# Optimization experiments

Measured on AMD Instinct MI355X. Metric: run time of the kernel, lower is better.

The kernel has to match this reference:

```python
import jax, jax.numpy as jnp
import numpy as np

N = 20000          # nodes
E = 200000         # edges
IN = 256           # in_channels
OUT = 256          # out_channels (heads * per-head)
H = 2              # heads
C = OUT // 2       # per-head channels (out_channels // 2)
TDIM = 100         # time_enc.out_channels
MSG = 156          # msg_dim
EDGE_DIM = TDIM + MSG  # 256
P = 0.1            # dropout prob


def setup_inputs() -> dict:
    key = jax.random.key(0)
    ks = jax.random.split(key, 20)
    s = 1.0 / np.sqrt(IN)
    se = 1.0 / np.sqrt(EDGE_DIM)
    return {
        "x": jax.random.normal(ks[0], (N, IN), jnp.float32),
        "last_update": jax.random.uniform(ks[1], (N,), jnp.float32) * 100.0,
        "edge_index": jax.random.randint(ks[2], (2, E), 0, N, jnp.int64),
        "t": jax.random.uniform(ks[3], (E,), jnp.float32) * 100.0,
        "msg": jax.random.normal(ks[4], (E, MSG), jnp.float32),
        "u_edge": jax.random.uniform(ks[5], (E,), jnp.float32),
        "u_attn": jax.random.uniform(ks[6], (E, H), jnp.float32),
        # TimeEncoder: cos(Linear(1, TDIM))
        "time_w": jax.random.normal(ks[7], (TDIM,), jnp.float32),
        "time_b": jax.random.normal(ks[8], (TDIM,), jnp.float32) * 0.1,
        # TransformerConv params ([in, out] layout)
        "Wq": jax.random.normal(ks[9], (IN, H * C), jnp.float32) * s,
        "bq": jnp.zeros((H * C,), jnp.float32),
        "Wk": jax.random.normal(ks[10], (IN, H * C), jnp.float32) * s,
        "bk": jnp.zeros((H * C,), jnp.float32),
        "Wv": jax.random.normal(ks[11], (IN, H * C), jnp.float32) * s,
        "bv": jnp.zeros((H * C,), jnp.float32),
        "We": jax.random.normal(ks[12], (EDGE_DIM, H * C), jnp.float32) * se,
        "be": jnp.zeros((H * C,), jnp.float32),
        "Ws": jax.random.normal(ks[13], (IN, H * C), jnp.float32) * s,
        "bs": jnp.zeros((H * C,), jnp.float32),
    }


def reference(x, last_update, edge_index, t, msg, u_edge, u_attn,
              time_w, time_b, Wq, bq, Wk, bk, Wv, bv, We, be, Ws, bs):
    src, dst = edge_index[0], edge_index[1]
    # time encoding of relative time (TGN TimeEncoder: cos(Linear(1, TDIM)))
    rel_t = last_update[src] - t                              # [E]
    rel_enc = jnp.cos(rel_t[:, None] * time_w[None, :] + time_b)  # [E, TDIM]
    edge_attr = jnp.concatenate([rel_enc, msg], axis=-1)      # [E, EDGE_DIM]
    # dropout_adj: drop edges with prob P (no rescale)
    keep = u_edge > P                                         # [E] bool

    q = (x @ Wq + bq).reshape(N, H, C)
    k = (x @ Wk + bk).reshape(N, H, C)
    v = (x @ Wv + bv).reshape(N, H, C)
    e = (edge_attr @ We + be).reshape(E, H, C)

    kj = k[src] + e                                           # [E, H, C]
    alpha = jnp.einsum('ehc,ehc->eh', q[dst], kj) / jnp.sqrt(jnp.float32(C))
    alpha = jnp.where(keep[:, None], alpha, -jnp.inf)
    # segment softmax over incoming edges of each dst node
    m = jax.ops.segment_max(alpha, dst, num_segments=N)       # [N, H]
    m = jnp.where(jnp.isfinite(m), m, 0.0)
    ex = jnp.where(keep[:, None], jnp.exp(alpha - m[dst]), 0.0)
    denom = jax.ops.segment_sum(ex, dst, num_segments=N)      # [N, H]
    attn = ex / (denom[dst] + 1e-16)                          # [E, H]
    # attention dropout (post-softmax, inverted scaling)
    attn = attn * (u_attn > P).astype(attn.dtype) / (1.0 - P)

    msg_out = (v[src] + e) * attn[:, :, None]                 # [E, H, C]
    out = jax.ops.segment_sum(msg_out, dst, num_segments=N).reshape(N, H * C)
    # root/skip connection
    return out + (x @ Ws + bs)
```

## Files before the change

### kernel.cpp

```cpp
#include <hip/hip_runtime.h>

#define NND 20000
#define NE 200000
#define PDROP 0.1f

typedef unsigned short u16;
typedef __bf16 bf16x8 __attribute__((ext_vector_type(8)));
typedef float f32x4 __attribute__((ext_vector_type(4)));

__device__ __forceinline__ float b2f(u16 u) {
  unsigned v = ((unsigned)u) << 16;
  float f;
  __builtin_memcpy(&f, &v, 4);
  return f;
}
__device__ __forceinline__ u16 f2b(float f) {
  unsigned x;
  __builtin_memcpy(&x, &f, 4);
  unsigned r = x + 0x7fffu + ((x >> 16) & 1u);
  return (u16)(r >> 16);
}

struct WTArgs {
  const float* W[6];
  u16* WT[6];
};

__global__ __launch_bounds__(256) void prep(const float* __restrict__ x,
                                            u16* __restrict__ xb, WTArgs a,
                                            int* __restrict__ cnt,
                                            int* __restrict__ cur) {
  const int b = blockIdx.x, tid = threadIdx.x;
  if (b < 5000) {
    int i = b * 256 + tid;
    float4 v = ((const float4*)x)[i];
    ushort4 o;
    o.x = f2b(v.x); o.y = f2b(v.y); o.z = f2b(v.z); o.w = f2b(v.w);
    ((ushort4*)xb)[i] = o;
  } else if (b < 6536) {
    int gid = (b - 5000) * 256 + tid;
    int w = gid >> 16, r = gid & 65535;
    if (w < 5) {
      int n = r >> 8, k = r & 255;
      a.WT[w][n * 256 + k] = f2b(a.W[w][k * 256 + n]);
    } else {
      a.WT[5][r] = f2b(a.W[5][r]);
    }
  } else {
    int i = (b - 6536) * 256 + tid;
    if (i < NND) { cnt[i] = 0; cur[i] = 0; }
  }
}

__global__ void csr_count(const int* __restrict__ ei, int* __restrict__ cnt) {
  int e = blockIdx.x * blockDim.x + threadIdx.x;
  if (e < NE) atomicAdd(&cnt[ei[NE + e]], 1);
}
__global__ __launch_bounds__(1024) void scan_rowptr(const int* __restrict__ cnt,
                                                    int* __restrict__ rowptr) {
  __shared__ int sums[1024];
  const int tid = threadIdx.x;
  const int base = tid * 20;
  int local[20];
  int run = 0;
#pragma unroll
  for (int i = 0; i < 20; i++) {
    int idx = base + i;
    local[i] = run;
    run += (idx < NND) ? cnt[idx] : 0;
  }
  sums[tid] = run;
  __syncthreads();
  for (int off = 1; off < 1024; off <<= 1) {
    int v = (tid >= off) ? sums[tid - off] : 0;
    __syncthreads();
    sums[tid] += v;
    __syncthreads();
  }
  int prev = (tid > 0) ? sums[tid - 1] : 0;
#pragma unroll
  for (int i = 0; i < 20; i++) {
    int idx = base + i;
    if (idx < NND) rowptr[idx] = prev + local[i];
  }
  if (tid == 1023) rowptr[NND] = sums[1023];
}

__global__ __launch_bounds__(256) void csr_fill(
    const int* __restrict__ ei, const float* __restrict__ last_update,
    const float* __restrict__ t, const float* __restrict__ u_edge,
    const float* __restrict__ u_attn, const float* __restrict__ msg,
    const int* __restrict__ rowptr, int* __restrict__ cur,
    uint4* __restrict__ recs, u16* __restrict__ msgs) {
  int e = (blockIdx.x * blockDim.x + threadIdx.x) >> 6;
  int lane = threadIdx.x & 63;
  if (e >= NE) return;
  int p = 0;
  if (lane == 0) {
    int s = ei[e];
    int d = ei[NE + e];
    p = rowptr[d] + atomicAdd(&cur[d], 1);
    bool keep = u_edge[e] > PDROP;
    float rt = last_update[s] - t[e];
    float2 ua = *(const float2*)&u_attn[(size_t)e * 2];
    uint4 r;
    r.x = (unsigned)s | (keep ? 0u : 0x80000000u);
    r.y = __float_as_uint(rt);
    r.z = __float_as_uint(ua.x > PDROP ? (1.f / 0.9f) : 0.f);
    r.w = __float_as_uint(ua.y > PDROP ? (1.f / 0.9f) : 0.f);
    recs[p] = r;
  }
  p = __shfl(p, 0);
  int c = lane * 4;
  if (c < 156) {
    float4 v = *(const float4*)&msg[(size_t)e * 156 + c];
    ushort4 o;
    o.x = f2b(v.x); o.y = f2b(v.y); o.z = f2b(v.z); o.w = f2b(v.w);
    *(ushort4*)&msgs[(size_t)p * 156 + c] = o;
  }
}

__device__ __forceinline__ void mfma_tile(const u16 (*As)[72], const u16 (*Bs)[72],
                                          f32x4 acc[4][4], int wm, int wn,
                                          int fr, int fg) {
#pragma unroll
  for (int ks = 0; ks < 2; ks++) {
    bf16x8 a[4], b[4];
#pragma unroll
    for (int i = 0; i < 4; i++)
      a[i] = *(const bf16x8*)&As[wm * 64 + i * 16 + fr][ks * 32 + fg * 8];
#pragma unroll
    for (int j = 0; j < 4; j++)
      b[j] = *(const bf16x8*)&Bs[wn * 64 + j * 16 + fr][ks * 32 + fg * 8];
#pragma unroll
    for (int i = 0; i < 4; i++)
#pragma unroll
      for (int j = 0; j < 4; j++)
        acc[i][j] = __builtin_amdgcn_mfma_f32_16x16x32_bf16(a[i], b[j], acc[i][j], 0, 0, 0);
  }
}

struct NodeArgs {
  const u16* BT[4];
  const float* bias[4];
  u16* outb[3];
  float* outf;
};
__global__ __launch_bounds__(256) void gemm_node(const u16* __restrict__ xb,
                                                 NodeArgs args) {
  __shared__ __attribute__((aligned(16))) u16 As[128][72];
  __shared__ __attribute__((aligned(16))) u16 Bs[128][72];
  const int tid = threadIdx.x;
  const int w = blockIdx.y >> 1;
  const int col0 = (blockIdx.y & 1) * 128;
  const int row0 = blockIdx.x * 128;
  const u16* BT = args.BT[w];
  const float* bias = args.bias[w];
  const int wid = tid >> 6, lane = tid & 63;
  const int wm = wid >> 1, wn = wid & 1;
  const int fr = lane & 15, fg = lane >> 4;
  f32x4 acc[4][4] = {};
  for (int k0 = 0; k0 < 256; k0 += 64) {
#pragma unroll
    for (int i = 0; i < 4; i++) {
      int idx = tid + i * 256;
      int row = idx >> 3, vc = idx & 7;
      int g = row0 + row;
      uint4 v = make_uint4(0, 0, 0, 0);
      if (g < NND) v = *(const uint4*)&xb[(size_t)g * 256 + k0 + vc * 8];
      *(uint4*)&As[row][vc * 8] = v;
      *(uint4*)&Bs[row][vc * 8] = *(const uint4*)&BT[(size_t)(col0 + row) * 256 + k0 + vc * 8];
    }
    __syncthreads();
    mfma_tile(As, Bs, acc, wm, wn, fr, fg);
    __syncthreads();
  }
#pragma unroll
  for (int mi = 0; mi < 4; mi++) {
#pragma unroll
    for (int rr = 0; rr < 4; rr++) {
      int grow = row0 + wm * 64 + mi * 16 + fg * 4 + rr;
      if (grow >= NND) continue;
#pragma unroll
      for (int ni = 0; ni < 4; ni++) {
        int gcol = col0 + wn * 64 + ni * 16 + fr;
        float val = acc[mi][ni][rr] + bias[gcol];
        if (w < 3)
          args.outb[w][(size_t)grow * 256 + gcol] = f2b(val);
        else
          args.outf[(size_t)grow * 256 + gcol] = val;
      }
    }
  }
}

__global__ __launch_bounds__(256) void gemm_qwe(const u16* __restrict__ qb,
                                                const u16* __restrict__ Web,
                                                u16* __restrict__ qWeb) {
  __shared__ __attribute__((aligned(16))) u16 As[128][72];
  __shared__ __attribute__((aligned(16))) u16 Bs[128][72];
  const int tid = threadIdx.x;
  const int h = blockIdx.y >> 1;
  const int col0 = (blockIdx.y & 1) * 128;
  const int row0 = blockIdx.x * 128;
  const int wid = tid >> 6, lane = tid & 63;
  const int wm = wid >> 1, wn = wid & 1;
  const int fr = lane & 15, fg = lane >> 4;
  f32x4 acc[4][4] = {};
  for (int k0 = 0; k0 < 128; k0 += 64) {
#pragma unroll
    for (int i = 0; i < 4; i++) {
      int idx = tid + i * 256;
      int row = idx >> 3, vc = idx & 7;
      int g = row0 + row;
      uint4 v = make_uint4(0, 0, 0, 0);
      if (g < NND) v = *(const uint4*)&qb[(size_t)g * 256 + h * 128 + k0 + vc * 8];
      *(uint4*)&As[row][vc * 8] = v;
      *(uint4*)&Bs[row][vc * 8] =
          *(const uint4*)&Web[(size_t)(col0 + row) * 256 + h * 128 + k0 + vc * 8];
    }
    __syncthreads();
    mfma_tile(As, Bs, acc, wm, wn, fr, fg);
    __syncthreads();
  }
#pragma unroll
  for (int mi = 0; mi < 4; mi++) {
#pragma unroll
    for (int rr = 0; rr < 4; rr++) {
      int grow = row0 + wm * 64 + mi * 16 + fg * 4 + rr;
      if (grow >= NND) continue;
#pragma unroll
      for (int ni = 0; ni < 4; ni++) {
        int gj = col0 + wn * 64 + ni * 16 + fr;
        qWeb[(size_t)grow * 512 + h * 256 + gj] = f2b(acc[mi][ni][rr]);
      }
    }
  }
}

__global__ __launch_bounds__(256) void node_fused(
    const u16* __restrict__ qb, const u16* __restrict__ kb,
    const u16* __restrict__ vb, const u16* __restrict__ qWeb,
    const u16* __restrict__ msgs, const float* __restrict__ tw,
    const float* __restrict__ tb_, const float* __restrict__ be,
    const int* __restrict__ rowptr, const uint4* __restrict__ recs,
    u16* __restrict__ aggb, float* __restrict__ out) {
  const int node = (blockIdx.x * blockDim.x + threadIdx.x) >> 6;
  const int lane = threadIdx.x & 63;
  if (node >= NND) return;
  const int beg = rowptr[node], end = rowptr[node + 1];
  const int c0 = lane * 4, hl = lane >> 5;

  ushort4 q4 = *(const ushort4*)&qb[(size_t)node * 256 + c0];
  float qf0 = b2f(q4.x), qf1 = b2f(q4.y), qf2 = b2f(q4.z), qf3 = b2f(q4.w);
  ushort4 w0v = *(const ushort4*)&qWeb[(size_t)node * 512 + c0];
  ushort4 w1v = *(const ushort4*)&qWeb[(size_t)node * 512 + 256 + c0];
  float qw00 = b2f(w0v.x), qw01 = b2f(w0v.y), qw02 = b2f(w0v.z), qw03 = b2f(w0v.w);
  float qw10 = b2f(w1v.x), qw11 = b2f(w1v.y), qw12 = b2f(w1v.z), qw13 = b2f(w1v.w);
  float4 bev = *(const float4*)&be[c0];
  float pb = qf0 * bev.x + qf1 * bev.y + qf2 * bev.z + qf3 * bev.w;
#pragma unroll
  for (int off = 16; off; off >>= 1) pb += __shfl_xor(pb, off);
  float tw0 = 0, tw1 = 0, tw2 = 0, tw3 = 0, tb0 = 0, tb1 = 0, tb2 = 0, tb3 = 0;
  if (c0 < 100) {
    float4 a = *(const float4*)&tw[c0];
    float4 b = *(const float4*)&tb_[c0];
    tw0 = a.x; tw1 = a.y; tw2 = a.z; tw3 = a.w;
    tb0 = b.x; tb1 = b.y; tb2 = b.z; tb3 = b.w;
  }
  const float inv = 0.08838834764831845f;

  float m0 = -INFINITY, m1 = -INFINITY;
  float den0 = 0.f, den1 = 0.f, sw0 = 0.f, sw1 = 0.f;
  float vc0 = 0, vc1 = 0, vc2 = 0, vc3 = 0;
  float g00 = 0, g01 = 0, g02 = 0, g03 = 0;
  float g10 = 0, g11 = 0, g12 = 0, g13 = 0;

  for (int j0 = beg; j0 < end; j0 += 4) {
    float ea[4][4];
    unsigned se[4];
    float rt[4], wk0[4], wk1[4];
    ushort4 k4[4], v4[4], mm4[4];
#pragma unroll
    for (int e = 0; e < 4; ++e) {
      int j = j0 + e;
      int jc = (j < end) ? j : (end - 1);
      uint4 rr = recs[jc];
      bool valid = (j < end);
      se[e] = valid ? rr.x : 0xFFFFFFFFu;
      rt[e] = __uint_as_float(rr.y);
      wk0[e] = valid ? __uint_as_float(rr.z) : 0.f;
      wk1[e] = valid ? __uint_as_float(rr.w) : 0.f;
      int s_ = (int)(rr.x & 0x7fffffffu);
      k4[e] = *(const ushort4*)&kb[(size_t)s_ * 256 + c0];
      v4[e] = *(const ushort4*)&vb[(size_t)s_ * 256 + c0];
      if (c0 >= 100)
        mm4[e] = *(const ushort4*)&msgs[(size_t)jc * 156 + (c0 - 100)];
    }
    if (c0 < 100) {
#pragma unroll
      for (int e = 0; e < 4; ++e) {
        ea[e][0] = __cosf(rt[e] * tw0 + tb0);
        ea[e][1] = __cosf(rt[e] * tw1 + tb1);
        ea[e][2] = __cosf(rt[e] * tw2 + tb2);
        ea[e][3] = __cosf(rt[e] * tw3 + tb3);
      }
    } else {
#pragma unroll
      for (int e = 0; e < 4; ++e) {
        ea[e][0] = b2f(mm4[e].x); ea[e][1] = b2f(mm4[e].y);
        ea[e][2] = b2f(mm4[e].z); ea[e][3] = b2f(mm4[e].w);
      }
    }
    float zq[4];
#pragma unroll
    for (int e = 0; e < 4; ++e) {
      float pq = qf0 * b2f(k4[e].x) + qf1 * b2f(k4[e].y) +
                 qf2 * b2f(k4[e].z) + qf3 * b2f(k4[e].w);
      float pe0 = qw00 * ea[e][0] + qw01 * ea[e][1] + qw02 * ea[e][2] + qw03 * ea[e][3];
      float pe1 = qw10 * ea[e][0] + qw11 * ea[e][1] + qw12 * ea[e][2] + qw13 * ea[e][3];
      float y0 = pe0 + __shfl_xor(pe0, 32);
      float y1 = pe1 + __shfl_xor(pe1, 32);
      zq[e] = ((lane < 32) ? y0 : y1) + pq;
    }
#pragma unroll
    for (int off = 16; off; off >>= 1) {
#pragma unroll
      for (int e = 0; e < 4; ++e) zq[e] += __shfl_xor(zq[e], off);
    }
    float a0[4], a1[4];
#pragma unroll
    for (int e = 0; e < 4; ++e) {
      float a = (se[e] < 0x80000000u) ? (zq[e] + pb) * inv : -INFINITY;
      float aoth = __shfl_xor(a, 32);
      a0[e] = (lane < 32) ? a : aoth;
      a1[e] = (lane < 32) ? aoth : a;
    }
    float cm0 = fmaxf(fmaxf(a0[0], a0[1]), fmaxf(a0[2], a0[3]));
    float cm1 = fmaxf(fmaxf(a1[0], a1[1]), fmaxf(a1[2], a1[3]));
    if (cm0 > m0) {
      float sc = (m0 > -1e30f) ? __expf(m0 - cm0) : 0.f;
      den0 *= sc; sw0 *= sc;
      g00 *= sc; g01 *= sc; g02 *= sc; g03 *= sc;
      float scv = hl ? 1.f : sc;
      vc0 *= scv; vc1 *= scv; vc2 *= scv; vc3 *= scv;
      m0 = cm0;
    }
    if (cm1 > m1) {
      float sc = (m1 > -1e30f) ? __expf(m1 - cm1) : 0.f;
      den1 *= sc; sw1 *= sc;
      g10 *= sc; g11 *= sc; g12 *= sc; g13 *= sc;
      float scv = hl ? sc : 1.f;
      vc0 *= scv; vc1 *= scv; vc2 *= scv; vc3 *= scv;
      m1 = cm1;
    }
#pragma unroll
    for (int e = 0; e < 4; ++e) {
      float ex0 = (a0[e] > -1e30f) ? __expf(a0[e] - m0) : 0.f;
      float ex1 = (a1[e] > -1e30f) ? __expf(a1[e] - m1) : 0.f;
      den0 += ex0; den1 += ex1;
      float w0 = ex0 * wk0[e], w1 = ex1 * wk1[e];
      float wv = hl ? w1 : w0;
      vc0 += wv * b2f(v4[e].x); vc1 += wv * b2f(v4[e].y);
      vc2 += wv * b2f(v4[e].z); vc3 += wv * b2f(v4[e].w);
      g00 += w0 * ea[e][0]; g01 += w0 * ea[e][1];
      g02 += w0 * ea[e][2]; g03 += w0 * ea[e][3];
      g10 += w1 * ea[e][0]; g11 += w1 * ea[e][1];
      g12 += w1 * ea[e][2]; g13 += w1 * ea[e][3];
      sw0 += w0; sw1 += w1;
    }
  }

  float rden0 = 1.f / (den0 + 1e-16f), rden1 = 1.f / (den1 + 1e-16f);
  float rv = hl ? rden1 : rden0;
  float swv = hl ? sw1 : sw0;
  float4 o = *(float4*)&out[(size_t)node * 256 + c0];
  o.x += (vc0 + swv * bev.x) * rv;
  o.y += (vc1 + swv * bev.y) * rv;
  o.z += (vc2 + swv * bev.z) * rv;
  o.w += (vc3 + swv * bev.w) * rv;
  *(float4*)&out[(size_t)node * 256 + c0] = o;
  ushort4 a0v, a1v;
  a0v.x = f2b(g00 * rden0); a0v.y = f2b(g01 * rden0);
  a0v.z = f2b(g02 * rden0); a0v.w = f2b(g03 * rden0);
  a1v.x = f2b(g10 * rden1); a1v.y = f2b(g11 * rden1);
  a1v.z = f2b(g12 * rden1); a1v.w = f2b(g13 * rden1);
  *(ushort4*)&aggb[(size_t)node * 256 + c0] = a0v;
  *(ushort4*)&aggb[(size_t)(NND + node) * 256 + c0] = a1v;
}

__global__ __launch_bounds__(256) void gemm_final(const u16* __restrict__ aggb,
                                                  const u16* __restrict__ WeT,
                                                  float* __restrict__ out) {
  __shared__ __attribute__((aligned(16))) u16 As[128][72];
  __shared__ __attribute__((aligned(16))) u16 Bs[128][72];
  const int tid = threadIdx.x;
  const int h = blockIdx.y;
  const int row0 = blockIdx.x * 128;
  const u16* A = aggb + (size_t)h * NND * 256;
  const int wid = tid >> 6, lane = tid & 63;
  const int wm = wid >> 1, wn = wid & 1;
  const int fr = lane & 15, fg = lane >> 4;
  f32x4 acc[4][4] = {};
  for (int k0 = 0; k0 < 256; k0 += 64) {
#pragma unroll
    for (int i = 0; i < 4; i++) {
      int idx = tid + i * 256;
      int row = idx >> 3, vc = idx & 7;
      int g = row0 + row;
      uint4 v = make_uint4(0, 0, 0, 0);
      if (g < NND) v = *(const uint4*)&A[(size_t)g * 256 + k0 + vc * 8];
      *(uint4*)&As[row][vc * 8] = v;
      *(uint4*)&Bs[row][vc * 8] =
          *(const uint4*)&WeT[(size_t)(h * 128 + row) * 256 + k0 + vc * 8];
    }
    __syncthreads();
    mfma_tile(As, Bs, acc, wm, wn, fr, fg);
    __syncthreads();
  }
#pragma unroll
  for (int mi = 0; mi < 4; mi++) {
#pragma unroll
    for (int rr = 0; rr < 4; rr++) {
      int grow = row0 + wm * 64 + mi * 16 + fg * 4 + rr;
      if (grow >= NND) continue;
#pragma unroll
      for (int ni = 0; ni < 4; ni++) {
        int gcol = wn * 64 + ni * 16 + fr;
        out[(size_t)grow * 256 + h * 128 + gcol] += acc[mi][ni][rr];
      }
    }
  }
}

extern "C" void kernel_launch(void* const* d_in, const int* in_sizes, int n_in,
                              void* d_out, int out_size, void* d_ws, size_t ws_size,
                              hipStream_t stream) {
  const float* x = (const float*)d_in[0];
  const float* last_update = (const float*)d_in[1];
  const int* ei = (const int*)d_in[2];
  const float* t = (const float*)d_in[3];
  const float* msg = (const float*)d_in[4];
  const float* u_edge = (const float*)d_in[5];
  const float* u_attn = (const float*)d_in[6];
  const float* time_w = (const float*)d_in[7];
  const float* time_b = (const float*)d_in[8];
  const float* Wq = (const float*)d_in[9];
  const float* bq = (const float*)d_in[10];
  const float* Wk = (const float*)d_in[11];
  const float* bk = (const float*)d_in[12];
  const float* Wv = (const float*)d_in[13];
  const float* bv = (const float*)d_in[14];
  const float* We = (const float*)d_in[15];
  const float* be = (const float*)d_in[16];
  const float* Ws = (const float*)d_in[17];
  const float* bs = (const float*)d_in[18];
  float* out = (float*)d_out;

  char* ws = (char*)d_ws;
  u16* xb = (u16*)(ws + 0);
  u16* WT0 = (u16*)(ws + 10240000);
  u16* qb = (u16*)(ws + 11026432);
  u16* kb = (u16*)(ws + 21266432);
  u16* vb = (u16*)(ws + 31506432);
  u16* qWeb = (u16*)(ws + 41746432);
  u16* aggb = (u16*)(ws + 62226432);
  uint4* recs = (uint4*)(ws + 82706432);
  u16* msgs = (u16*)(ws + 85906432);
  int* cnt = (int*)(ws + 148306432);
  int* cur = (int*)(ws + 148386432);
  int* rowptr = (int*)(ws + 148466432);

  WTArgs wa;
  wa.W[0] = Wq; wa.W[1] = Wk; wa.W[2] = Wv; wa.W[3] = Ws; wa.W[4] = We; wa.W[5] = We;
  for (int i = 0; i < 6; i++) wa.WT[i] = WT0 + (size_t)i * 65536;
  prep<<<6615, 256, 0, stream>>>(x, xb, wa, cnt, cur);

  csr_count<<<(NE + 255) / 256, 256, 0, stream>>>(ei, cnt);
  scan_rowptr<<<1, 1024, 0, stream>>>(cnt, rowptr);
  csr_fill<<<NE / 4, 256, 0, stream>>>(ei, last_update, t, u_edge, u_attn, msg,
                                       rowptr, cur, recs, msgs);

  NodeArgs na;
  na.BT[0] = wa.WT[0]; na.BT[1] = wa.WT[1]; na.BT[2] = wa.WT[2]; na.BT[3] = wa.WT[3];
  na.bias[0] = bq; na.bias[1] = bk; na.bias[2] = bv; na.bias[3] = bs;
  na.outb[0] = qb; na.outb[1] = kb; na.outb[2] = vb;
  na.outf = out;
  dim3 gn((NND + 127) / 128, 8);
  gemm_node<<<gn, 256, 0, stream>>>(xb, na);

  dim3 gq((NND + 127) / 128, 4);
  gemm_qwe<<<gq, 256, 0, stream>>>(qb, wa.WT[5], qWeb);

  node_fused<<<(NND + 3) / 4, 256, 0, stream>>>(
      qb, kb, vb, qWeb, msgs, time_w, time_b, be, rowptr, recs, aggb, out);

  dim3 gf((NND + 127) / 128, 2);
  gemm_final<<<gf, 256, 0, stream>>>(aggb, wa.WT[4], out);
}
```

Measured before the change: 268.5 us.

## Fold Wq·We into combined weight and convert msg in edge order

Precomputes Wq_h·We_h^T (and bq·We) as a combined weight so q·We is produced directly from x inside the node GEMM, removing the separate gemm_qwe kernel that depended on q. The msg bf16 conversion moves into a coalesced prep pass in original edge order, and the CSR records now carry the edge id so node_fused gathers msg rows by edge id. This cuts the one-warp-per-edge csr_fill scatter but makes msg reads in node_fused random instead of sequential, and adds a small weight-product kernel.

```diff
diff --git a/kernel.cpp b/kernel.cpp
--- a/kernel.cpp
+++ b/kernel.cpp
@@ -22,33 +22,62 @@
 }
 
 struct WTArgs {
-  const float* W[6];
-  u16* WT[6];
+  const float* W[5];
+  u16* WT[5];
 };
 
 __global__ __launch_bounds__(256) void prep(const float* __restrict__ x,
                                             u16* __restrict__ xb, WTArgs a,
+                                            const float* __restrict__ msg,
+                                            u16* __restrict__ msgb,
                                             int* __restrict__ cnt,
                                             int* __restrict__ cur) {
   const int b = blockIdx.x, tid = threadIdx.x;
-  if (b < 5000) {
+  if (b < 30469) {
     int i = b * 256 + tid;
+    if (i < 7800000) {
+      float4 v = ((const float4*)msg)[i];
+      ushort4 o;
+      o.x = f2b(v.x); o.y = f2b(v.y); o.z = f2b(v.z); o.w = f2b(v.w);
+      ((ushort4*)msgb)[i] = o;
+    }
+  } else if (b < 35469) {
+    int i = (b - 30469) * 256 + tid;
     float4 v = ((const float4*)x)[i];
     ushort4 o;
     o.x = f2b(v.x); o.y = f2b(v.y); o.z = f2b(v.z); o.w = f2b(v.w);
     ((ushort4*)xb)[i] = o;
-  } else if (b < 6536) {
-    int gid = (b - 5000) * 256 + tid;
+  } else if (b < 36749) {
+    int gid = (b - 35469) * 256 + tid;
     int w = gid >> 16, r = gid & 65535;
-    if (w < 5) {
-      int n = r >> 8, k = r & 255;
-      a.WT[w][n * 256 + k] = f2b(a.W[w][k * 256 + n]);
-    } else {
-      a.WT[5][r] = f2b(a.W[5][r]);
-    }
+    int n = r >> 8, k = r & 255;
+    a.WT[w][n * 256 + k] = f2b(a.W[w][k * 256 + n]);
   } else {
-    int i = (b - 6536) * 256 + tid;
+    int i = (b - 36749) * 256 + tid;
     if (i < NND) { cnt[i] = 0; cur[i] = 0; }
+  }
+}
+
+__global__ void wprep(const float* __restrict__ Wq, const float* __restrict__ We,
+                      const float* __restrict__ bq, u16* __restrict__ WcT,
+                      float* __restrict__ qwe_bias) {
+  int gid = blockIdx.x * blockDim.x + threadIdx.x;
+  if (gid < 131072) {
+    int i = gid & 255, j = gid >> 8;
+    int h = j >> 8, jj = j & 255;
+    float acc = 0.f;
+#pragma unroll 4
+    for (int c = 0; c < 128; c++)
+      acc += Wq[i * 256 + h * 128 + c] * We[jj * 256 + h * 128 + c];
+    WcT[j * 256 + i] = f2b(acc);
+  } else if (gid < 131584) {
+    int j = gid - 131072;
+    int h = j >> 8, jj = j & 255;
+    float acc = 0.f;
+#pragma unroll 4
+    for (int c = 0; c < 128; c++)
+      acc += bq[h * 128 + c] * We[jj * 256 + h * 128 + c];
+    qwe_bias[j] = acc;
   }
 }
 
@@ -86,37 +115,28 @@
   if (tid == 1023) rowptr[NND] = sums[1023];
 }
 
-__global__ __launch_bounds__(256) void csr_fill(
-    const int* __restrict__ ei, const float* __restrict__ last_update,
-    const float* __restrict__ t, const float* __restrict__ u_edge,
-    const float* __restrict__ u_attn, const float* __restrict__ msg,
-    const int* __restrict__ rowptr, int* __restrict__ cur,
-    uint4* __restrict__ recs, u16* __restrict__ msgs) {
-  int e = (blockIdx.x * blockDim.x + threadIdx.x) >> 6;
-  int lane = threadIdx.x & 63;
-  if (e >= NE) return;
-  int p = 0;
-  if (lane == 0) {
+__global__ void csr_fill(const int* __restrict__ ei,
+                         const float* __restrict__ last_update,
+                         const float* __restrict__ t,
+                         const float* __restrict__ u_edge,
+                         const float* __restrict__ u_attn,
+                         const int* __restrict__ rowptr, int* __restrict__ cur,
+                         uint4* __restrict__ recs) {
+  int e = blockIdx.x * blockDim.x + threadIdx.x;
+  if (e < NE) {
     int s = ei[e];
     int d = ei[NE + e];
-    p = rowptr[d] + atomicAdd(&cur[d], 1);
+    int p = rowptr[d] + atomicAdd(&cur[d], 1);
     bool keep = u_edge[e] > PDROP;
     float rt = last_update[s] - t[e];
     float2 ua = *(const float2*)&u_attn[(size_t)e * 2];
     uint4 r;
     r.x = (unsigned)s | (keep ? 0u : 0x80000000u);
     r.y = __float_as_uint(rt);
-    r.z = __float_as_uint(ua.x > PDROP ? (1.f / 0.9f) : 0.f);
-    r.w = __float_as_uint(ua.y > PDROP ? (1.f / 0.9f) : 0.f);
+    r.z = (unsigned)e | ((ua.x > PDROP) ? 0x40000000u : 0u) |
+          ((ua.y > PDROP) ? 0x80000000u : 0u);
+    r.w = 0u;
     recs[p] = r;
-  }
-  p = __shfl(p, 0);
-  int c = lane * 4;
-  if (c < 156) {
-    float4 v = *(const float4*)&msg[(size_t)e * 156 + c];
-    ushort4 o;
-    o.x = f2b(v.x); o.y = f2b(v.y); o.z = f2b(v.z); o.w = f2b(v.w);
-    *(ushort4*)&msgs[(size_t)p * 156 + c] = o;
   }
 }
 
@@ -141,10 +161,11 @@
 }
 
 struct NodeArgs {
-  const u16* BT[4];
-  const float* bias[4];
+  const u16* BT[6];
+  const float* bias[6];
   u16* outb[3];
   float* outf;
+  u16* qWeb;
 };
 __global__ __launch_bounds__(256) void gemm_node(const u16* __restrict__ xb,
                                                  NodeArgs args) {
@@ -187,52 +208,10 @@
         float val = acc[mi][ni][rr] + bias[gcol];
         if (w < 3)
           args.outb[w][(size_t)grow * 256 + gcol] = f2b(val);
+        else if (w == 3)
+          args.outf[(size_t)grow * 256 + gcol] = val;
         else
-          args.outf[(size_t)grow * 256 + gcol] = val;
-      }
-    }
-  }
-}
-
-__global__ __launch_bounds__(256) void gemm_qwe(const u16* __restrict__ qb,
-                                                const u16* __restrict__ Web,
-                                                u16* __restrict__ qWeb) {
-  __shared__ __attribute__((aligned(16))) u16 As[128][72];
-  __shared__ __attribute__((aligned(16))) u16 Bs[128][72];
-  const int tid = threadIdx.x;
-  const int h = blockIdx.y >> 1;
-  const int col0 = (blockIdx.y & 1) * 128;
-  const int row0 = blockIdx.x * 128;
-  const int wid = tid >> 6, lane = tid & 63;
-  const int wm = wid >> 1, wn = wid & 1;
-  const int fr = lane & 15, fg = lane >> 4;
-  f32x4 acc[4][4] = {};
-  for (int k0 = 0; k0 < 128; k0 += 64) {
-#pragma unroll
-    for (int i = 0; i < 4; i++) {
-      int idx = tid + i * 256;
-      int row = idx >> 3, vc = idx & 7;
-      int g = row0 + row;
-      uint4 v = make_uint4(0, 0, 0, 0);
-      if (g < NND) v = *(const uint4*)&qb[(size_t)g * 256 + h * 128 + k0 + vc * 8];
-      *(uint4*)&As[row][vc * 8] = v;
-      *(uint4*)&Bs[row][vc * 8] =
-          *(const uint4*)&Web[(size_t)(col0 + row) * 256 + h * 128 + k0 + vc * 8];
-    }
-    __syncthreads();
-    mfma_tile(As, Bs, acc, wm, wn, fr, fg);
-    __syncthreads();
-  }
-#pragma unroll
-  for (int mi = 0; mi < 4; mi++) {
-#pragma unroll
-    for (int rr = 0; rr < 4; rr++) {
-      int grow = row0 + wm * 64 + mi * 16 + fg * 4 + rr;
-      if (grow >= NND) continue;
-#pragma unroll
-      for (int ni = 0; ni < 4; ni++) {
-        int gj = col0 + wn * 64 + ni * 16 + fr;
-        qWeb[(size_t)grow * 512 + h * 256 + gj] = f2b(acc[mi][ni][rr]);
+          args.qWeb[(size_t)grow * 512 + (w - 4) * 256 + gcol] = f2b(val);
       }
     }
   }
@@ -241,7 +220,7 @@
 __global__ __launch_bounds__(256) void node_fused(
     const u16* __restrict__ qb, const u16* __restrict__ kb,
     const u16* __restrict__ vb, const u16* __restrict__ qWeb,
-    const u16* __restrict__ msgs, const float* __restrict__ tw,
+    const u16* __restrict__ msgb, const float* __restrict__ tw,
     const float* __restrict__ tb_, const float* __restrict__ be,
     const int* __restrict__ rowptr, const uint4* __restrict__ recs,
     u16* __restrict__ aggb, float* __restrict__ out) {
@@ -289,13 +268,16 @@
       bool valid = (j < end);
       se[e] = valid ? rr.x : 0xFFFFFFFFu;
       rt[e] = __uint_as_float(rr.y);
-      wk0[e] = valid ? __uint_as_float(rr.z) : 0.f;
-      wk1[e] = valid ? __uint_as_float(rr.w) : 0.f;
+      unsigned rz = rr.z;
+      wk0[e] = (valid && (rz & 0x40000000u)) ? (1.f / 0.9f) : 0.f;
+      wk1[e] = (valid && (rz & 0x80000000u)) ? (1.f / 0.9f) : 0.f;
       int s_ = (int)(rr.x & 0x7fffffffu);
       k4[e] = *(const ushort4*)&kb[(size_t)s_ * 256 + c0];
       v4[e] = *(const ushort4*)&vb[(size_t)s_ * 256 + c0];
-      if (c0 >= 100)
-        mm4[e] = *(const ushort4*)&msgs[(size_t)jc * 156 + (c0 - 100)];
+      if (c0 >= 100) {
+        int eid = (int)(rz & 0x3FFFFFFFu);
+        mm4[e] = *(const ushort4*)&msgb[(size_t)eid * 156 + (c0 - 100)];
+      }
     }
     if (c0 < 100) {
 #pragma unroll
@@ -460,40 +442,44 @@
   char* ws = (char*)d_ws;
   u16* xb = (u16*)(ws + 0);
   u16* WT0 = (u16*)(ws + 10240000);
-  u16* qb = (u16*)(ws + 11026432);
-  u16* kb = (u16*)(ws + 21266432);
-  u16* vb = (u16*)(ws + 31506432);
-  u16* qWeb = (u16*)(ws + 41746432);
-  u16* aggb = (u16*)(ws + 62226432);
-  uint4* recs = (uint4*)(ws + 82706432);
-  u16* msgs = (u16*)(ws + 85906432);
-  int* cnt = (int*)(ws + 148306432);
-  int* cur = (int*)(ws + 148386432);
-  int* rowptr = (int*)(ws + 148466432);
+  u16* WcT = (u16*)(ws + 10895360);
+  float* qwe_bias = (float*)(ws + 11157504);
+  u16* qb = (u16*)(ws + 11159552);
+  u16* kb = (u16*)(ws + 21399552);
+  u16* vb = (u16*)(ws + 31639552);
+  u16* qWeb = (u16*)(ws + 41879552);
+  u16* aggb = (u16*)(ws + 62359552);
+  uint4* recs = (uint4*)(ws + 82839552);
+  u16* msgb = (u16*)(ws + 86039552);
+  int* cnt = (int*)(ws + 148439552);
+  int* cur = (int*)(ws + 148519552);
+  int* rowptr = (int*)(ws + 148599552);
 
   WTArgs wa;
-  wa.W[0] = Wq; wa.W[1] = Wk; wa.W[2] = Wv; wa.W[3] = Ws; wa.W[4] = We; wa.W[5] = We;
-  for (int i = 0; i < 6; i++) wa.WT[i] = WT0 + (size_t)i * 65536;
-  prep<<<6615, 256, 0, stream>>>(x, xb, wa, cnt, cur);
+  wa.W[0] = Wq; wa.W[1] = Wk; wa.W[2] = Wv; wa.W[3] = Ws; wa.W[4] = We;
+  for (int i = 0; i < 5; i++) wa.WT[i] = WT0 + (size_t)i * 65536;
+  prep<<<36828, 256, 0, stream>>>(x, xb, wa, msg, msgb, cnt, cur);
+
+  wprep<<<514, 256, 0, stream>>>(Wq, We, bq, WcT, qwe_bias);
 
   csr_count<<<(NE + 255) / 256, 256, 0, stream>>>(ei, cnt);
   scan_rowptr<<<1, 1024, 0, stream>>>(cnt, rowptr);
-  csr_fill<<<NE / 4, 256, 0, stream>>>(ei, last_update, t, u_edge, u_attn, msg,
-                                       rowptr, cur, recs, msgs);
+  csr_fill<<<(NE + 255) / 256, 256, 0, stream>>>(ei, last_update, t, u_edge,
+                                                 u_attn, rowptr, cur, recs);
 
   NodeArgs na;
   na.BT[0] = wa.WT[0]; na.BT[1] = wa.WT[1]; na.BT[2] = wa.WT[2]; na.BT[3] = wa.WT[3];
+  na.BT[4] = WcT; na.BT[5] = WcT + 256 * 256;
   na.bias[0] = bq; na.bias[1] = bk; na.bias[2] = bv; na.bias[3] = bs;
+  na.bias[4] = qwe_bias; na.bias[5] = qwe_bias + 256;
   na.outb[0] = qb; na.outb[1] = kb; na.outb[2] = vb;
   na.outf = out;
-  dim3 gn((NND + 127) / 128, 8);
+  na.qWeb = qWeb;
+  dim3 gn((NND + 127) / 128, 12);
   gemm_node<<<gn, 256, 0, stream>>>(xb, na);
 
-  dim3 gq((NND + 127) / 128, 4);
-  gemm_qwe<<<gq, 256, 0, stream>>>(qb, wa.WT[5], qWeb);
-
   node_fused<<<(NND + 3) / 4, 256, 0, stream>>>(
-      qb, kb, vb, qWeb, msgs, time_w, time_b, be, rowptr, recs, aggb, out);
+      qb, kb, vb, qWeb, msgb, time_w, time_b, be, rowptr, recs, aggb, out);
 
   dim3 gf((NND + 127) / 128, 2);
   gemm_final<<<gf, 256, 0, stream>>>(aggb, wa.WT[4], out);
```

Measured after the change: 265.8 us. Within noise of the previous version (-1.0%).
